# Kernel optimization log

Measured on AMD Instinct MI355X. Metric: run time of the kernel, lower is better.

The kernel has to match this reference:

```python
import jax, jax.numpy as jnp
import numpy as np
from jax import lax

B, N, T, HOR, HID = 512, 128, 128, 32, 512


def _uni(k, shape, s):
    return jax.random.uniform(k, shape, jnp.float32, -s, s)


def setup_inputs() -> dict:
    key = jax.random.key(0)
    ks = jax.random.split(key, 24)
    s = 1.0 / np.sqrt(HID)
    inp = {"window": jax.random.normal(ks[0], (B * N, T), jnp.float32)}
    # encoder LSTM (2 layers, torch gate order i,f,g,o)
    inp["Wih0"] = _uni(ks[1], (4 * HID, N), s); inp["Whh0"] = _uni(ks[2], (4 * HID, HID), s)
    inp["bih0"] = _uni(ks[3], (4 * HID,), s);   inp["bhh0"] = _uni(ks[4], (4 * HID,), s)
    inp["Wih1"] = _uni(ks[5], (4 * HID, HID), s); inp["Whh1"] = _uni(ks[6], (4 * HID, HID), s)
    inp["bih1"] = _uni(ks[7], (4 * HID,), s);     inp["bhh1"] = _uni(ks[8], (4 * HID,), s)
    # decoder cells
    inp["Wc1i"] = _uni(ks[9], (4 * HID, N), s);   inp["Wc1h"] = _uni(ks[10], (4 * HID, HID), s)
    inp["bc1i"] = _uni(ks[11], (4 * HID,), s);    inp["bc1h"] = _uni(ks[12], (4 * HID,), s)
    inp["Wc2i"] = _uni(ks[13], (4 * HID, HID), s); inp["Wc2h"] = _uni(ks[14], (4 * HID, HID), s)
    inp["bc2i"] = _uni(ks[15], (4 * HID,), s);     inp["bc2h"] = _uni(ks[16], (4 * HID,), s)
    # output projection
    inp["Wp"] = _uni(ks[17], (N, HID), s); inp["bp"] = _uni(ks[18], (N,), s)
    # deterministic inverted-dropout masks
    keep_e = 0.75  # nn.LSTM inter-layer dropout p=0.25
    keep_d = 0.8   # F.dropout p=0.2 in decode loop
    inp["enc_mask"] = (jax.random.uniform(ks[19], (T, B, HID)) < keep_e).astype(jnp.float32) / keep_e
    inp["dec_h_mask"] = (jax.random.uniform(ks[20], (HOR - 1, B, HID)) < keep_d).astype(jnp.float32) / keep_d
    inp["dec_c_mask"] = (jax.random.uniform(ks[21], (HOR - 1, B, HID)) < keep_d).astype(jnp.float32) / keep_d
    return inp


def _cell(x, h, c, Wih, Whh, bih, bhh):
    g = x @ Wih.T + h @ Whh.T + (bih + bhh)
    i, f, gg, o = jnp.split(g, 4, axis=-1)
    c = jax.nn.sigmoid(f) * c + jax.nn.sigmoid(i) * jnp.tanh(gg)
    h = jax.nn.sigmoid(o) * jnp.tanh(c)
    return h, c


def _run_layer(xs, Wih, Whh, bih, bhh):
    # xs: [T, B, D] -> outputs [T, B, HID], final (h, c)
    h0 = jnp.zeros((xs.shape[1], HID), xs.dtype)
    def step(carry, x):
        h, c = carry
        h, c = _cell(x, h, c, Wih, Whh, bih, bhh)
        return (h, c), h
    (h, c), hs = lax.scan(step, (h0, h0), xs)
    return hs, h, c


def reference(window, Wih0, Whh0, bih0, bhh0, Wih1, Whh1, bih1, bhh1,
              Wc1i, Wc1h, bc1i, bc1h, Wc2i, Wc2h, bc2i, bc2h, Wp, bp,
              enc_mask, dec_h_mask, dec_c_mask):
    x = window.reshape(B, T, N).transpose(1, 0, 2)  # [T, B, N]
    hs0, h1, c1 = _run_layer(x, Wih0, Whh0, bih0, bhh0)
    hs0 = hs0 * enc_mask  # inter-layer dropout (training mode)
    _, h2, c2 = _run_layer(hs0, Wih1, Whh1, bih1, bhh1)

    def dec_step(carry, masks):
        h1, c1, h2, c2 = carry
        mh, mc = masks
        pred = h2 @ Wp.T + bp                       # [B, N]
        h1, c1 = _cell(pred, h1, c1, Wc1i, Wc1h, bc1i, bc1h)
        h1 = h1 * mh
        c1 = c1 * mc
        h2, c2 = _cell(h1, h2, c2, Wc2i, Wc2h, bc2i, bc2h)
        return (h1, c1, h2, c2), pred

    (h1, c1, h2, c2), preds = lax.scan(dec_step, (h1, c1, h2, c2), (dec_h_mask, dec_c_mask))
    final = h2 @ Wp.T + bp                          # [B, N]
    allp = jnp.concatenate([preds, final[None]], axis=0)  # [HOR, B, N]
    # torch: each pred.view(-1,1), cat dim=1 -> [B*N, HOR]
    return allp.transpose(1, 2, 0).reshape(B * N, HOR)
```

## Files before the change

kernel.cpp:

```cpp
#include <hip/hip_runtime.h>
#include <math.h>

#define HID 512
#define BAT 512
#define NIN 128
#define TST 128
#define HOR 32
#define SBZ ((size_t)BAT * HID)
#define SL 262144
#define SLB 524288

using bf16x8 = __attribute__((ext_vector_type(8))) __bf16;
using f32x4  = __attribute__((ext_vector_type(4))) float;

__device__ __forceinline__ float sigf(float x) { return 1.0f / (1.0f + __expf(-x)); }
__device__ __forceinline__ float tanhfast(float x) { return 1.0f - 2.0f / (__expf(2.0f * x) + 1.0f); }

__device__ __forceinline__ short f2bf(float x) {
    union { float f; unsigned u; } v; v.f = x;
    unsigned r = (v.u + 0x7FFFu + ((v.u >> 16) & 1u)) >> 16;
    return (short)r;
}
__device__ __forceinline__ float bf2f(short s) {
    union { unsigned u; float f; } v; v.u = ((unsigned)(unsigned short)s) << 16;
    return v.f;
}
__device__ __forceinline__ bf16x8 asbf(f32x4 v) {
    union { f32x4 f; bf16x8 b; } u; u.f = v; return u.b;
}

__device__ __forceinline__ void pbar(unsigned* b, int sub, unsigned ep) {
    __syncthreads();
    if (threadIdx.x == 0) {
        unsigned* leaf = b + (sub >> 3) * 32;
        unsigned* root = b + 512;
        unsigned* flag = b + 544;
        unsigned old = __hip_atomic_fetch_add(leaf, 1u, __ATOMIC_RELAXED, __HIP_MEMORY_SCOPE_AGENT);
        if (old == 8u * ep - 1u) {
            unsigned ro = __hip_atomic_fetch_add(root, 1u, __ATOMIC_RELAXED, __HIP_MEMORY_SCOPE_AGENT);
            if (ro == 8u * ep - 1u)
                __hip_atomic_store(flag, ep, __ATOMIC_RELAXED, __HIP_MEMORY_SCOPE_AGENT);
        }
        int spin = 0;
        while (__hip_atomic_load(flag, __ATOMIC_RELAXED, __HIP_MEMORY_SCOPE_AGENT) < ep) {
            __builtin_amdgcn_s_sleep(1);
            if (((++spin) & 63) == 0)
                __hip_atomic_fetch_add(flag, 0u, __ATOMIC_RELAXED, __HIP_MEMORY_SCOPE_AGENT);
        }
    }
    __syncthreads();
}

__device__ __forceinline__ void gbar3(unsigned* bar, int bid, unsigned ep) {
    __syncthreads();
    if (threadIdx.x == 0) {
        unsigned* leaf = bar + ((unsigned)bid >> 3) * 32;
        unsigned* root = bar + 1024;
        unsigned* flag = bar + 1056;
        unsigned old = __hip_atomic_fetch_add(leaf, 1u, __ATOMIC_RELAXED, __HIP_MEMORY_SCOPE_AGENT);
        if (old == 8u * ep - 1u) {
            unsigned ro = __hip_atomic_fetch_add(root, 1u, __ATOMIC_RELAXED, __HIP_MEMORY_SCOPE_AGENT);
            if (ro == 32u * ep - 1u)
                __hip_atomic_store(flag, ep, __ATOMIC_RELAXED, __HIP_MEMORY_SCOPE_AGENT);
        }
        int spin = 0;
        while (__hip_atomic_load(flag, __ATOMIC_RELAXED, __HIP_MEMORY_SCOPE_AGENT) < ep) {
            __builtin_amdgcn_s_sleep(1);
            if (((++spin) & 63) == 0)
                __hip_atomic_fetch_add(flag, 0u, __ATOMIC_RELAXED, __HIP_MEMORY_SCOPE_AGENT);
        }
    }
    __syncthreads();
}


__global__ __launch_bounds__(256) void prep_w(const float* __restrict__ Wih,
                                              const float* __restrict__ Whh,
                                              short* __restrict__ W2, int Kx, int Kp) {
    size_t i = (size_t)blockIdx.x * 256 + threadIdx.x;
    if (i >= (size_t)2048 * Kp) return;
    int np = (int)(i / Kp), kp = (int)(i % Kp);
    int u = np >> 2, gate = np & 3;
    int on = gate * HID + u;
    float w = (kp < Kx) ? Wih[(size_t)on * Kx + kp] : Whh[(size_t)on * HID + (kp - Kx)];
    W2[i] = f2bf(w);
}

__global__ __launch_bounds__(256) void prep_x(const float* __restrict__ window,
                                              short* __restrict__ X2t) {
    size_t i = (size_t)blockIdx.x * 256 + threadIdx.x;
    if (i >= (size_t)TST * BAT * NIN) return;
    int n = (int)(i & 127);
    int b = (int)((i >> 7) & 511);
    int t = (int)(i >> 16);
    float x = window[(size_t)b * (TST * NIN) + (size_t)t * NIN + n];
    int rg = b >> 4;
    int l = (b & 15) + (((n >> 3) & 3) << 4);
    int e = n & 7;
    size_t base = (size_t)t * 65536 + ((size_t)(rg * 4 + (n >> 5)) << 9) + l * 8 + e;
    X2t[base] = f2bf(x);
}

__global__ __launch_bounds__(256) void prep_fuse(const float* __restrict__ Wc1i,
                                                 const float* __restrict__ Wp,
                                                 float* __restrict__ Wfuse) {
    size_t i = (size_t)blockIdx.x * 256 + threadIdx.x;
    if (i >= (size_t)2048 * 512) return;
    int on = (int)(i >> 9), k = (int)(i & 511);
    float s = 0.f;
    for (int n = 0; n < NIN; ++n) s += Wc1i[(size_t)on * NIN + n] * Wp[(size_t)n * HID + k];
    Wfuse[i] = s;
}

__global__ __launch_bounds__(256) void prep_badd(const float* __restrict__ Wc1i,
                                                 const float* __restrict__ bp,
                                                 float* __restrict__ badd) {
    int on = blockIdx.x * 256 + threadIdx.x;
    if (on >= 2048) return;
    float s = 0.f;
    for (int n = 0; n < NIN; ++n) s += Wc1i[(size_t)on * NIN + n] * bp[n];
    badd[on] = s;
}

__global__ __launch_bounds__(256) void prep_bias(const float* __restrict__ bih,
                                                 const float* __restrict__ bhh,
                                                 const float* __restrict__ badd,
                                                 float* __restrict__ bout) {
    int np = blockIdx.x * 256 + threadIdx.x;
    if (np >= 2048) return;
    int on = (np & 3) * HID + (np >> 2);
    float v = bih[on] + bhh[on];
    if (badd) v += badd[on];
    bout[np] = v;
}

__global__ __launch_bounds__(256) void prep_wp(const float* __restrict__ Wp,
                                               short* __restrict__ W2p) {
    int i = blockIdx.x * 256 + threadIdx.x;
    if (i >= 128 * 512) return;
    W2p[i] = f2bf(Wp[i]);
}


template<bool SC>
__device__ __forceinline__ void gl16(f32x4& q, const char* p) {
    if constexpr (SC)
        asm volatile("global_load_dwordx4 %0, %1, off sc0 sc1" : "=v"(q) : "v"(p));
    else
        asm volatile("global_load_dwordx4 %0, %1, off" : "=v"(q) : "v"(p));
}

__device__ __forceinline__ void load_wres32(char* lds, const short* Wg, int K) {
    const int tid = threadIdx.x;
    const int r = tid >> 4;
    const int cnt = K >> 7;
    const int jb = (tid & 15) * cnt;
    for (int q = 0; q < cnt; ++q) {
        int j = jb + q;
        bf16x8 v = *(const bf16x8*)(Wg + (size_t)r * K + j * 8);
        *(bf16x8*)(lds + j * 512 + r * 16) = v;
    }
}

__device__ __forceinline__ void load_wres64(char* lds, const short* Wg, int K) {
    const int r = threadIdx.x >> 2, jg = threadIdx.x & 3;
    for (int q = 0; q < (K >> 5); ++q) {
        int j = jg + (q << 2);
        bf16x8 v = *(const bf16x8*)(Wg + (size_t)r * K + j * 8);
        *(bf16x8*)(lds + (size_t)j * 1024 + r * 16) = v;
    }
}

__device__ __forceinline__ void pre_mask_asm(const float* msk, int mrow, int u0, float o[4]) {
    const int lane = threadIdx.x & 63;
    const float* p = msk + (size_t)(mrow + ((lane >> 3) << 2)) * HID + u0 + (lane & 7);
#pragma unroll
    for (int r = 0; r < 4; ++r)
        asm volatile("global_load_dword %0, %1, off" : "=v"(o[r]) : "v"(p + (size_t)r * HID));
}

template<int C0, int C1, bool SC0, bool SC1>
__device__ __forceinline__ void gemm64(
    const char* wres, const short* a0t, const short* a1t,
    int mb, f32x4 acc[2][4])
{
    constexpr int NKC = C0 + C1;
    constexpr int D = 16;
    const int lane = threadIdx.x & 63;
    const int arow = lane & 15, akg = lane >> 4;
    const size_t lb = (size_t)lane << 4;
    const char* base0 = (const char*)a0t;
    const char* base1 = (const char*)a1t;
    auto cptr = [&](int kc, int fh) -> const char* {
        return (kc < C0)
            ? base0 + (((size_t)(mb * 2 + fh) * C0 + kc) << 10) + lb
            : base1 + (((size_t)(mb * 2 + fh) * C1 + (kc - C0)) << 10) + lb;
    };
    f32x4 q0[D], q1[D];
#pragma unroll
    for (int i = 0; i < D; ++i) {
        if (i < C0) { gl16<SC0>(q0[i], cptr(i, 0)); gl16<SC0>(q1[i], cptr(i, 1)); }
        else        { gl16<SC1>(q0[i], cptr(i, 0)); gl16<SC1>(q1[i], cptr(i, 1)); }
    }
#pragma unroll
    for (int kc = 0; kc < NKC; ++kc) {
        const int sl = kc % D;
        asm volatile("s_waitcnt vmcnt(%2)"
                     : "+v"(q0[sl]), "+v"(q1[sl])
                     : "i"((2 * ((NKC - kc) < D ? (NKC - kc) : D)) - 2));
        const bf16x8 fa0 = asbf(q0[sl]);
        const bf16x8 fa1 = asbf(q1[sl]);
        if (kc + D < NKC) {
            if (kc + D < C0) { gl16<SC0>(q0[sl], cptr(kc + D, 0)); gl16<SC0>(q1[sl], cptr(kc + D, 1)); }
            else             { gl16<SC1>(q0[sl], cptr(kc + D, 0)); gl16<SC1>(q1[sl], cptr(kc + D, 1)); }
        }
        const char* wrow = wres + (size_t)((kc << 2) + akg) * 1024;
        bf16x8 fb[4];
#pragma unroll
        for (int nj = 0; nj < 4; ++nj)
            fb[nj] = *(const bf16x8*)(wrow + ((nj * 16 + arow) << 4));
#pragma unroll
        for (int nj = 0; nj < 4; ++nj) {
            acc[0][nj] = __builtin_amdgcn_mfma_f32_16x16x32_bf16(fa0, fb[nj], acc[0][nj], 0, 0, 0);
            acc[1][nj] = __builtin_amdgcn_mfma_f32_16x16x32_bf16(fa1, fb[nj], acc[1][nj], 0, 0, 0);
        }
    }
    asm volatile("s_waitcnt vmcnt(0)");
}

__device__ __forceinline__ void cell_epi64(
    char* scrw, f32x4 acc[2][4], float creg[2][4], int mb, int np0,
    const float* bias_p, const float* mh, const float* mc, const float* ma,
    short* h_out, short* h_aux)
{
    const int lane = threadIdx.x & 63;
#pragma unroll
    for (int p = 0; p < 2; ++p) {
        const int np0p = np0 + (p << 5);
#pragma unroll
        for (int mi = 0; mi < 2; ++mi)
#pragma unroll
            for (int nj = 0; nj < 2; ++nj) {
                const int row = mi * 16 + ((lane >> 4) << 2);
                const int col = nj * 16 + (lane & 15);
#pragma unroll
                for (int r = 0; r < 4; ++r)
                    *(float*)(scrw + (row + r) * 128 + (col << 2)) = acc[mi][p * 2 + nj][r];
            }
        asm volatile("s_waitcnt lgkmcnt(0)" ::: "memory");
        const int ul = lane & 7, g = lane >> 3;
        f32x4 gv[4];
#pragma unroll
        for (int r = 0; r < 4; ++r)
            gv[r] = *(const f32x4*)(scrw + ((g << 2) + r) * 128 + (ul << 4));
        asm volatile("s_waitcnt lgkmcnt(0)" ::: "memory");
        const float4 bs = *(const float4*)(bias_p + np0p + (ul << 2));
#pragma unroll
        for (int r = 0; r < 4; ++r) {
            const int m = (g << 2) + r;
            const int fh = m >> 4, r16 = m & 15;
            const float gi = gv[r][0] + bs.x, gf = gv[r][1] + bs.y;
            const float gg = gv[r][2] + bs.z, go = gv[r][3] + bs.w;
            const float cn = sigf(gf) * creg[p][r] + sigf(gi) * tanhfast(gg);
            const float h  = sigf(go) * tanhfast(cn);
            creg[p][r] = mc ? cn * mc[p * 4 + r] : cn;
            const float hm = mh ? h * mh[p * 4 + r] : h;
            const int idx2 = (r16 << 3) + ul;
            *(short*)(scrw + fh * 256 + idx2 * 2) = f2bf(hm);
            if (h_aux)
                *(short*)(scrw + 512 + fh * 256 + idx2 * 2) = f2bf(h * ma[p * 4 + r]);
        }
        const int u0p = np0p >> 2;
        const int c_hi = u0p >> 5, gsub = (u0p >> 3) & 3;
        unsigned vmain[2], vaux[2];
#pragma unroll
        for (int s = 0; s < 2; ++s)
            vmain[s] = *(const unsigned*)(scrw + s * 256 + (lane << 2));
        if (h_aux)
#pragma unroll
            for (int s = 0; s < 2; ++s)
                vaux[s] = *(const unsigned*)(scrw + 512 + s * 256 + (lane << 2));
        asm volatile("s_waitcnt lgkmcnt(0)" ::: "memory");
#pragma unroll
        for (int s = 0; s < 2; ++s) {
            const unsigned* dst = (const unsigned*)(h_out
                + ((size_t)((mb * 2 + s) * 16 + c_hi) << 9) + (gsub << 7)) + lane;
            asm volatile("global_store_dword %0, %1, off sc0 sc1" :: "v"(dst), "v"(vmain[s]));
        }
        if (h_aux)
#pragma unroll
            for (int s = 0; s < 2; ++s) {
                const unsigned* dst = (const unsigned*)(h_aux
                    + ((size_t)((mb * 2 + s) * 16 + c_hi) << 9) + (gsub << 7)) + lane;
                asm volatile("global_store_dword %0, %1, off sc0 sc1" :: "v"(dst), "v"(vaux[s]));
            }
    }
}


__global__ void __launch_bounds__(256, 1) persist_kernel(
    const short* __restrict__ X2t,
    const short* __restrict__ W0, const short* __restrict__ W1,
    const short* __restrict__ Wd1, const short* __restrict__ Wd2,
    short* hA0, short* hA1, short* hd0, short* hd1, short* hB0, short* hB1,
    short* hBall0, short* hBallR,
    const float* __restrict__ bias0, const float* __restrict__ bias1,
    const float* __restrict__ biasd1, const float* __restrict__ biasd2,
    const float* __restrict__ enc_mask, const float* __restrict__ dec_h_mask,
    const float* __restrict__ dec_c_mask, unsigned* bar)
{
    extern __shared__ __align__(16) char lds[];
    const int bid = blockIdx.x;
    const int xcd = bid & 7;
    const int half = xcd >> 2;
    const int mtile = xcd & 3;
    const int m0 = mtile * 128;
    const int ntile = bid >> 3;
    const int np0 = ntile * 64;
    const int u0 = np0 >> 2;
    const int w = threadIdx.x >> 6;
    const int mb = (m0 >> 5) + w;
    const int mrow = m0 + (w << 5);
    char* scrw = lds + 131072 + (w << 12);
    float creg[2][4] = {{0.f,0.f,0.f,0.f},{0.f,0.f,0.f,0.f}};

    unsigned* pb = bar + mtile * 1024;
    unsigned* gb = bar + 4096;
    const int sub = (half << 5) | ntile;

    auto hA_rd = [&](int t) -> const short* { return (t & 1) ? hA1 : hA0; };
    auto hA_wr = [&](int t) -> short* { return (t & 1) ? hA0 : hA1; };
    auto hd_at = [&](int t) -> short* { return (t & 1) ? hd1 : hd0; };
    auto hB_rd = [&](int t) -> const short* { return (t & 1) ? hB1 : hB0; };
    auto hB_wr = [&](int t) -> short* { return (t & 1) ? hB0 : hB1; };
    auto decA_at = [&](int i) -> short* { return (i & 1) ? hA1 : hA0; };
    auto hball = [&](int i) -> short* { return (i == 0) ? hBall0 : hBallR + (size_t)(i - 1) * SL; };

    load_wres64(lds, (half ? W1 : W0) + (size_t)np0 * (half ? 1024 : 640), half ? 1024 : 640);
    __syncthreads();
    unsigned ep = 0;
    for (int tt = 0; tt <= TST; ++tt) {
        if (half == 0) {
            if (tt < TST) {
                const int t = tt;
                float ma[8];
                pre_mask_asm(enc_mask + (size_t)t * SBZ, mrow, u0, ma);
                pre_mask_asm(enc_mask + (size_t)t * SBZ, mrow, u0 + 8, ma + 4);
                f32x4 acc[2][4];
#pragma unroll
                for (int a = 0; a < 2; ++a)
#pragma unroll
                    for (int b2 = 0; b2 < 4; ++b2) acc[a][b2] = (f32x4){0.f, 0.f, 0.f, 0.f};
                gemm64<4, 16, false, true>(lds, X2t + (size_t)t * 65536, hA_rd(t), mb, acc);
                cell_epi64(scrw, acc, creg, mb, np0, bias0, nullptr, nullptr, ma,
                           hA_wr(t), hd_at(t));
            }
        } else {
            if (tt >= 1) {
                const int t = tt - 1;
                f32x4 acc[2][4];
#pragma unroll
                for (int a = 0; a < 2; ++a)
#pragma unroll
                    for (int b2 = 0; b2 < 4; ++b2) acc[a][b2] = (f32x4){0.f, 0.f, 0.f, 0.f};
                gemm64<16, 16, true, true>(lds, hd_at(t), hB_rd(t), mb, acc);
                short* outp = (t == TST - 1) ? hBall0 : hB_wr(t);
                cell_epi64(scrw, acc, creg, mb, np0, bias1, nullptr, nullptr, nullptr,
                           outp, nullptr);
            }
        }
        pbar(pb, sub, ++ep);
    }

    gbar3(gb, bid, 1u);

    load_wres64(lds, (half ? Wd2 : Wd1) + (size_t)np0 * 1024, 1024);
    __syncthreads();
    for (int s = 0; s < HOR - 1; ++s) {
        if (half == 0) {
            float mh[8], mc[8];
            pre_mask_asm(dec_h_mask + (size_t)s * SBZ, mrow, u0, mh);
            pre_mask_asm(dec_h_mask + (size_t)s * SBZ, mrow, u0 + 8, mh + 4);
            pre_mask_asm(dec_c_mask + (size_t)s * SBZ, mrow, u0, mc);
            pre_mask_asm(dec_c_mask + (size_t)s * SBZ, mrow, u0 + 8, mc + 4);
            f32x4 acc[2][4];
#pragma unroll
            for (int a = 0; a < 2; ++a)
#pragma unroll
                for (int b2 = 0; b2 < 4; ++b2) acc[a][b2] = (f32x4){0.f, 0.f, 0.f, 0.f};
            gemm64<16, 16, true, true>(lds, hball(s), decA_at(s), mb, acc);
            cell_epi64(scrw, acc, creg, mb, np0, biasd1, mh, mc, nullptr,
                       decA_at(s + 1), nullptr);
        }
        pbar(pb, sub, ++ep);
        if (half == 1) {
            f32x4 acc[2][4];
#pragma unroll
            for (int a = 0; a < 2; ++a)
#pragma unroll
                for (int b2 = 0; b2 < 4; ++b2) acc[a][b2] = (f32x4){0.f, 0.f, 0.f, 0.f};
            gemm64<16, 16, true, true>(lds, decA_at(s + 1), hball(s), mb, acc);
            cell_epi64(scrw, acc, creg, mb, np0, biasd2, nullptr, nullptr, nullptr,
                       hball(s + 1), nullptr);
        }
        pbar(pb, sub, ++ep);
    }
}


template<int C0, int C1>
__device__ __forceinline__ void gemm_pipeP(
    const char* wres, const short* a0t, const short* a1t,
    int mb, f32x4 acc[2][2])
{
    constexpr int NKC = C0 + C1;
    constexpr int D = 16;
    const int lane = threadIdx.x & 63;
    const int arow = lane & 15, akg = lane >> 4;
    const size_t lb = (size_t)lane << 4;
    const char* base0 = (const char*)a0t;
    const char* base1 = (const char*)a1t;
    auto cptr = [&](int kc, int fh) -> const char* {
        return (kc < C0)
            ? base0 + (((size_t)(mb * 2 + fh) * C0 + kc) << 10) + lb
            : base1 + (((size_t)(mb * 2 + fh) * C1 + (kc - C0)) << 10) + lb;
    };
    f32x4 q0[D], q1[D];
#pragma unroll
    for (int i = 0; i < D; ++i) {
        gl16<false>(q0[i], cptr(i, 0));
        gl16<false>(q1[i], cptr(i, 1));
    }
#pragma unroll
    for (int kc = 0; kc < NKC; ++kc) {
        const int sl = kc % D;
        asm volatile("s_waitcnt vmcnt(%2)"
                     : "+v"(q0[sl]), "+v"(q1[sl])
                     : "i"((2 * ((NKC - kc) < D ? (NKC - kc) : D)) - 2));
        const bf16x8 fa0 = asbf(q0[sl]);
        const bf16x8 fa1 = asbf(q1[sl]);
        if (kc + D < NKC) {
            gl16<false>(q0[sl], cptr(kc + D, 0));
            gl16<false>(q1[sl], cptr(kc + D, 1));
        }
        const char* wrow = wres + (size_t)(((kc << 2) + akg) << 9);
        const bf16x8 fb0 = *(const bf16x8*)(wrow + (arow << 4));
        const bf16x8 fb1 = *(const bf16x8*)(wrow + ((16 + arow) << 4));
        acc[0][0] = __builtin_amdgcn_mfma_f32_16x16x32_bf16(fa0, fb0, acc[0][0], 0, 0, 0);
        acc[0][1] = __builtin_amdgcn_mfma_f32_16x16x32_bf16(fa0, fb1, acc[0][1], 0, 0, 0);
        acc[1][0] = __builtin_amdgcn_mfma_f32_16x16x32_bf16(fa1, fb0, acc[1][0], 0, 0, 0);
        acc[1][1] = __builtin_amdgcn_mfma_f32_16x16x32_bf16(fa1, fb1, acc[1][1], 0, 0, 0);
    }
    asm volatile("s_waitcnt vmcnt(0)");
}

__global__ void __launch_bounds__(512, 2) proj_kernel(
    const short* hBall0, const short* hBallR, const short* __restrict__ W2p,
    const float* __restrict__ bp, float* __restrict__ pred_all)
{
    extern __shared__ __align__(16) char lds[];
    const int bid = blockIdx.x;
    const int s = bid >> 3, q = bid & 7;
    const int bh = q >> 2, n0p = (q & 3) * 32;
    load_wres32(lds, W2p + (size_t)n0p * 512, 512);
    const int w = threadIdx.x >> 6, lane = threadIdx.x & 63;
    char* scrw = lds + 32768 + w * 4608;
    const int mb = bh * 8 + w;
    const short* A = (s == 0) ? hBall0 : hBallR + (size_t)(s - 1) * SL;
    __syncthreads();
    f32x4 acc[2][2];
#pragma unroll
    for (int a = 0; a < 2; ++a)
#pragma unroll
        for (int b2 = 0; b2 < 2; ++b2) acc[a][b2] = (f32x4){0.f, 0.f, 0.f, 0.f};
    gemm_pipeP<16, 0>(lds, A, A, mb, acc);
#pragma unroll
    for (int mi = 0; mi < 2; ++mi)
#pragma unroll
        for (int ni = 0; ni < 2; ++ni) {
            const int row = mi * 16 + ((lane >> 4) << 2);
            const int col = ni * 16 + (lane & 15);
#pragma unroll
            for (int r = 0; r < 4; ++r)
                *(float*)(scrw + (row + r) * 144 + (col << 2)) = acc[mi][ni][r];
        }
    asm volatile("s_waitcnt lgkmcnt(0)" ::: "memory");
    const int rr = lane >> 1, hf = lane & 1;
    float* dst = pred_all + (size_t)s * (BAT * NIN)
               + (size_t)(bh * 256 + w * 32 + rr) * NIN + n0p + hf * 16;
#pragma unroll
    for (int t4 = 0; t4 < 4; ++t4) {
        f32x4 v = *(const f32x4*)(scrw + rr * 144 + hf * 64 + t4 * 16);
        const float4 b4 = *(const float4*)(bp + n0p + hf * 16 + t4 * 4);
        v[0] += b4.x; v[1] += b4.y; v[2] += b4.z; v[3] += b4.w;
        *(f32x4*)(dst + t4 * 4) = v;
    }
}

__global__ __launch_bounds__(256) void transpose_out(const float* __restrict__ pred_all,
                                                     float* __restrict__ out) {
    __shared__ float tl[32][65];
    const int base = blockIdx.x * 64;
    const int tid = threadIdx.x;
    for (int i = tid; i < 32 * 64; i += 256) {
        int s = i >> 6, f = i & 63;
        tl[s][f] = pred_all[(size_t)s * (BAT * NIN) + base + f];
    }
    __syncthreads();
    for (int i = tid; i < 64 * 32; i += 256) {
        int f = i >> 5, s = i & 31;
        out[(size_t)(base + f) * HOR + s] = tl[s][f];
    }
}


extern "C" void kernel_launch(void* const* d_in, const int* in_sizes, int n_in,
                              void* d_out, int out_size, void* d_ws, size_t ws_size,
                              hipStream_t stream) {
    (void)in_sizes; (void)n_in; (void)out_size; (void)ws_size;
    const float* window = (const float*)d_in[0];
    const float* Wih0 = (const float*)d_in[1];
    const float* Whh0 = (const float*)d_in[2];
    const float* bih0 = (const float*)d_in[3];
    const float* bhh0 = (const float*)d_in[4];
    const float* Wih1 = (const float*)d_in[5];
    const float* Whh1 = (const float*)d_in[6];
    const float* bih1 = (const float*)d_in[7];
    const float* bhh1 = (const float*)d_in[8];
    const float* Wc1i = (const float*)d_in[9];
    const float* Wc1h = (const float*)d_in[10];
    const float* bc1i = (const float*)d_in[11];
    const float* bc1h = (const float*)d_in[12];
    const float* Wc2i = (const float*)d_in[13];
    const float* Wc2h = (const float*)d_in[14];
    const float* bc2i = (const float*)d_in[15];
    const float* bc2h = (const float*)d_in[16];
    const float* Wp   = (const float*)d_in[17];
    const float* bp   = (const float*)d_in[18];
    const float* enc_mask   = (const float*)d_in[19];
    const float* dec_h_mask = (const float*)d_in[20];
    const float* dec_c_mask = (const float*)d_in[21];
    float* out = (float*)d_out;

    char* base = (char*)d_ws;
    size_t off = 0;
    auto take = [&](size_t bytes) -> char* {
        off = (off + 255) & ~(size_t)255;
        char* r = base + off; off += bytes; return r;
    };
    short* W2e0 = (short*)take((size_t)2048 * 640 * 2);
    short* W2e1 = (short*)take((size_t)2048 * 1024 * 2);
    short* W2d1 = (short*)take((size_t)2048 * 1024 * 2);
    short* W2d2 = (short*)take((size_t)2048 * 1024 * 2);
    short* W2p  = (short*)take((size_t)128 * 512 * 2);
    float* Wfuse = (float*)take((size_t)2048 * 512 * 4);
    float* badd  = (float*)take((size_t)2048 * 4);
    float* bias0 = (float*)take((size_t)2048 * 4);
    float* bias1 = (float*)take((size_t)2048 * 4);
    float* biasd1 = (float*)take((size_t)2048 * 4);
    float* biasd2 = (float*)take((size_t)2048 * 4);
    short* hBall0 = (short*)take(SLB);
    float* pred_all = (float*)take((size_t)HOR * BAT * NIN * 4);
    unsigned* bars = (unsigned*)take(32768);
    short* X2t = (short*)take((size_t)TST * 65536 * 2);
    short* hA0 = (short*)take(SLB);
    short* hA1 = (short*)take(SLB);
    short* hd0 = (short*)take(SLB);
    short* hd1 = (short*)take(SLB);
    short* hB0 = (short*)take(SLB);
    short* hB1 = (short*)take(SLB);
    short* hBallR = X2t;

    prep_fuse<<<(2048 * 512 + 255) / 256, 256, 0, stream>>>(Wc1i, Wp, Wfuse);
    prep_badd<<<8, 256, 0, stream>>>(Wc1i, bp, badd);
    prep_wp<<<(128 * 512 + 255) / 256, 256, 0, stream>>>(Wp, W2p);
    prep_w<<<(2048 * 640 + 255) / 256, 256, 0, stream>>>(Wih0, Whh0, W2e0, NIN, 640);
    prep_w<<<(2048 * 1024 + 255) / 256, 256, 0, stream>>>(Wih1, Whh1, W2e1, HID, 1024);
    prep_w<<<(2048 * 1024 + 255) / 256, 256, 0, stream>>>(Wfuse, Wc1h, W2d1, HID, 1024);
    prep_w<<<(2048 * 1024 + 255) / 256, 256, 0, stream>>>(Wc2i, Wc2h, W2d2, HID, 1024);
    prep_bias<<<8, 256, 0, stream>>>(bih0, bhh0, nullptr, bias0);
    prep_bias<<<8, 256, 0, stream>>>(bih1, bhh1, nullptr, bias1);
    prep_bias<<<8, 256, 0, stream>>>(bc1i, bc1h, badd, biasd1);
    prep_bias<<<8, 256, 0, stream>>>(bc2i, bc2h, nullptr, biasd2);
    prep_x<<<(int)(((size_t)TST * BAT * NIN + 255) / 256), 256, 0, stream>>>(window, X2t);
    hipMemsetAsync(hA0, 0, SLB, stream);
    hipMemsetAsync(hB0, 0, SLB, stream);
    hipMemsetAsync(bars, 0, 32768, stream);

    hipFuncSetAttribute((const void*)&persist_kernel,
                        hipFuncAttributeMaxDynamicSharedMemorySize, 163840);
    persist_kernel<<<256, 256, 147456, stream>>>(
        X2t, W2e0, W2e1, W2d1, W2d2,
        hA0, hA1, hd0, hd1, hB0, hB1,
        hBall0, hBallR,
        bias0, bias1, biasd1, biasd2,
        enc_mask, dec_h_mask, dec_c_mask, bars);

    hipFuncSetAttribute((const void*)&proj_kernel,
                        hipFuncAttributeMaxDynamicSharedMemorySize, 69632);
    proj_kernel<<<256, 512, 69632, stream>>>(hBall0, hBallR, W2p, bp, pred_all);

    transpose_out<<<(BAT * NIN) / 64, 256, 0, stream>>>(pred_all, out);
}
```

Baseline: 1.736 ms.

## Replace coherent hidden-state loads with 16-slot ring buffers and periodic acquire fences

Hidden-state buffers for the encoder and decoder are changed from double buffers to 16-deep ring buffers, so each step reads a fresh address. That lets the recurrent GEMM loads drop the sc0/sc1 cache-bypass bits and use normal cached loads. Coherence now comes from an agent-scope acquire fence issued once every 16 barrier epochs, which invalidates stale cache lines before any ring slot is reused. The cost is more memory footprint, and correctness depends on the fence cadence lining up with ring reuse.

```diff
diff --git a/kernel.cpp b/kernel.cpp
--- a/kernel.cpp
+++ b/kernel.cpp
@@ -142,12 +142,8 @@
 }
 
 
-template<bool SC>
-__device__ __forceinline__ void gl16(f32x4& q, const char* p) {
-    if constexpr (SC)
-        asm volatile("global_load_dwordx4 %0, %1, off sc0 sc1" : "=v"(q) : "v"(p));
-    else
-        asm volatile("global_load_dwordx4 %0, %1, off" : "=v"(q) : "v"(p));
+__device__ __forceinline__ void gl16c(f32x4& q, const char* p) {
+    asm volatile("global_load_dwordx4 %0, %1, off" : "=v"(q) : "v"(p));
 }
 
 __device__ __forceinline__ void load_wres32(char* lds, const short* Wg, int K) {
@@ -179,7 +175,7 @@
         asm volatile("global_load_dword %0, %1, off" : "=v"(o[r]) : "v"(p + (size_t)r * HID));
 }
 
-template<int C0, int C1, bool SC0, bool SC1>
+template<int C0, int C1>
 __device__ __forceinline__ void gemm64(
     const char* wres, const short* a0t, const short* a1t,
     int mb, f32x4 acc[2][4])
@@ -199,8 +195,8 @@
     f32x4 q0[D], q1[D];
 #pragma unroll
     for (int i = 0; i < D; ++i) {
-        if (i < C0) { gl16<SC0>(q0[i], cptr(i, 0)); gl16<SC0>(q1[i], cptr(i, 1)); }
-        else        { gl16<SC1>(q0[i], cptr(i, 0)); gl16<SC1>(q1[i], cptr(i, 1)); }
+        gl16c(q0[i], cptr(i, 0));
+        gl16c(q1[i], cptr(i, 1));
     }
 #pragma unroll
     for (int kc = 0; kc < NKC; ++kc) {
@@ -211,8 +207,8 @@
         const bf16x8 fa0 = asbf(q0[sl]);
         const bf16x8 fa1 = asbf(q1[sl]);
         if (kc + D < NKC) {
-            if (kc + D < C0) { gl16<SC0>(q0[sl], cptr(kc + D, 0)); gl16<SC0>(q1[sl], cptr(kc + D, 1)); }
-            else             { gl16<SC1>(q0[sl], cptr(kc + D, 0)); gl16<SC1>(q1[sl], cptr(kc + D, 1)); }
+            gl16c(q0[sl], cptr(kc + D, 0));
+            gl16c(q1[sl], cptr(kc + D, 1));
         }
         const char* wrow = wres + (size_t)((kc << 2) + akg) * 1024;
         bf16x8 fb[4];
@@ -302,7 +298,7 @@
     const short* __restrict__ X2t,
     const short* __restrict__ W0, const short* __restrict__ W1,
     const short* __restrict__ Wd1, const short* __restrict__ Wd2,
-    short* hA0, short* hA1, short* hd0, short* hd1, short* hB0, short* hB1,
+    short* hAring, short* hdring, short* hBring, short* decAring,
     short* hBall0, short* hBallR,
     const float* __restrict__ bias0, const float* __restrict__ bias1,
     const float* __restrict__ biasd1, const float* __restrict__ biasd2,
@@ -328,12 +324,14 @@
     unsigned* gb = bar + 4096;
     const int sub = (half << 5) | ntile;
 
-    auto hA_rd = [&](int t) -> const short* { return (t & 1) ? hA1 : hA0; };
-    auto hA_wr = [&](int t) -> short* { return (t & 1) ? hA0 : hA1; };
-    auto hd_at = [&](int t) -> short* { return (t & 1) ? hd1 : hd0; };
-    auto hB_rd = [&](int t) -> const short* { return (t & 1) ? hB1 : hB0; };
-    auto hB_wr = [&](int t) -> short* { return (t & 1) ? hB0 : hB1; };
-    auto decA_at = [&](int i) -> short* { return (i & 1) ? hA1 : hA0; };
+    auto hA_rd = [&](int t) -> const short* { return hAring + (size_t)(t & 15) * SL; };
+    auto hA_wr = [&](int t) -> short* { return hAring + (size_t)((t + 1) & 15) * SL; };
+    auto hd_at = [&](int t) -> short* { return hdring + (size_t)(t & 15) * SL; };
+    auto hB_rd = [&](int t) -> const short* { return hBring + (size_t)(t & 15) * SL; };
+    auto hB_wr = [&](int t) -> short* { return hBring + (size_t)((t + 1) & 15) * SL; };
+    auto decA_at = [&](int i) -> short* {
+        return (i == 0) ? hAring : decAring + (size_t)(i & 15) * SL;
+    };
     auto hball = [&](int i) -> short* { return (i == 0) ? hBall0 : hBallR + (size_t)(i - 1) * SL; };
 
     load_wres64(lds, (half ? W1 : W0) + (size_t)np0 * (half ? 1024 : 640), half ? 1024 : 640);
@@ -351,7 +349,7 @@
                 for (int a = 0; a < 2; ++a)
 #pragma unroll
                     for (int b2 = 0; b2 < 4; ++b2) acc[a][b2] = (f32x4){0.f, 0.f, 0.f, 0.f};
-                gemm64<4, 16, false, true>(lds, X2t + (size_t)t * 65536, hA_rd(t), mb, acc);
+                gemm64<4, 16>(lds, X2t + (size_t)t * 65536, hA_rd(t), mb, acc);
                 cell_epi64(scrw, acc, creg, mb, np0, bias0, nullptr, nullptr, ma,
                            hA_wr(t), hd_at(t));
             }
@@ -363,16 +361,19 @@
                 for (int a = 0; a < 2; ++a)
 #pragma unroll
                     for (int b2 = 0; b2 < 4; ++b2) acc[a][b2] = (f32x4){0.f, 0.f, 0.f, 0.f};
-                gemm64<16, 16, true, true>(lds, hd_at(t), hB_rd(t), mb, acc);
+                gemm64<16, 16>(lds, hd_at(t), hB_rd(t), mb, acc);
                 short* outp = (t == TST - 1) ? hBall0 : hB_wr(t);
                 cell_epi64(scrw, acc, creg, mb, np0, bias1, nullptr, nullptr, nullptr,
                            outp, nullptr);
             }
         }
         pbar(pb, sub, ++ep);
+        if ((ep & 15) == 2)
+            __builtin_amdgcn_fence(__ATOMIC_ACQUIRE, "agent");
     }
 
     gbar3(gb, bid, 1u);
+    __builtin_amdgcn_fence(__ATOMIC_ACQUIRE, "agent");
 
     load_wres64(lds, (half ? Wd2 : Wd1) + (size_t)np0 * 1024, 1024);
     __syncthreads();
@@ -388,22 +389,26 @@
             for (int a = 0; a < 2; ++a)
 #pragma unroll
                 for (int b2 = 0; b2 < 4; ++b2) acc[a][b2] = (f32x4){0.f, 0.f, 0.f, 0.f};
-            gemm64<16, 16, true, true>(lds, hball(s), decA_at(s), mb, acc);
+            gemm64<16, 16>(lds, hball(s), decA_at(s), mb, acc);
             cell_epi64(scrw, acc, creg, mb, np0, biasd1, mh, mc, nullptr,
                        decA_at(s + 1), nullptr);
         }
         pbar(pb, sub, ++ep);
+        if ((ep & 15) == 2)
+            __builtin_amdgcn_fence(__ATOMIC_ACQUIRE, "agent");
         if (half == 1) {
             f32x4 acc[2][4];
 #pragma unroll
             for (int a = 0; a < 2; ++a)
 #pragma unroll
                 for (int b2 = 0; b2 < 4; ++b2) acc[a][b2] = (f32x4){0.f, 0.f, 0.f, 0.f};
-            gemm64<16, 16, true, true>(lds, decA_at(s + 1), hball(s), mb, acc);
+            gemm64<16, 16>(lds, decA_at(s + 1), hball(s), mb, acc);
             cell_epi64(scrw, acc, creg, mb, np0, biasd2, nullptr, nullptr, nullptr,
                        hball(s + 1), nullptr);
         }
         pbar(pb, sub, ++ep);
+        if ((ep & 15) == 2)
+            __builtin_amdgcn_fence(__ATOMIC_ACQUIRE, "agent");
     }
 }
 
@@ -428,8 +433,8 @@
     f32x4 q0[D], q1[D];
 #pragma unroll
     for (int i = 0; i < D; ++i) {
-        gl16<false>(q0[i], cptr(i, 0));
-        gl16<false>(q1[i], cptr(i, 1));
+        gl16c(q0[i], cptr(i, 0));
+        gl16c(q1[i], cptr(i, 1));
     }
 #pragma unroll
     for (int kc = 0; kc < NKC; ++kc) {
@@ -440,8 +445,8 @@
         const bf16x8 fa0 = asbf(q0[sl]);
         const bf16x8 fa1 = asbf(q1[sl]);
         if (kc + D < NKC) {
-            gl16<false>(q0[sl], cptr(kc + D, 0));
-            gl16<false>(q1[sl], cptr(kc + D, 1));
+            gl16c(q0[sl], cptr(kc + D, 0));
+            gl16c(q1[sl], cptr(kc + D, 1));
         }
         const char* wrow = wres + (size_t)(((kc << 2) + akg) << 9);
         const bf16x8 fb0 = *(const bf16x8*)(wrow + (arow << 4));
@@ -563,12 +568,10 @@
     float* pred_all = (float*)take((size_t)HOR * BAT * NIN * 4);
     unsigned* bars = (unsigned*)take(32768);
     short* X2t = (short*)take((size_t)TST * 65536 * 2);
-    short* hA0 = (short*)take(SLB);
-    short* hA1 = (short*)take(SLB);
-    short* hd0 = (short*)take(SLB);
-    short* hd1 = (short*)take(SLB);
-    short* hB0 = (short*)take(SLB);
-    short* hB1 = (short*)take(SLB);
+    short* hAring  = (short*)take((size_t)16 * SLB);
+    short* hdring  = (short*)take((size_t)16 * SLB);
+    short* hBring  = (short*)take((size_t)16 * SLB);
+    short* decAring = (short*)take((size_t)16 * SLB);
     short* hBallR = X2t;
 
     prep_fuse<<<(2048 * 512 + 255) / 256, 256, 0, stream>>>(Wc1i, Wp, Wfuse);
@@ -583,15 +586,15 @@
     prep_bias<<<8, 256, 0, stream>>>(bc1i, bc1h, badd, biasd1);
     prep_bias<<<8, 256, 0, stream>>>(bc2i, bc2h, nullptr, biasd2);
     prep_x<<<(int)(((size_t)TST * BAT * NIN + 255) / 256), 256, 0, stream>>>(window, X2t);
-    hipMemsetAsync(hA0, 0, SLB, stream);
-    hipMemsetAsync(hB0, 0, SLB, stream);
+    hipMemsetAsync(hAring, 0, SLB, stream);
+    hipMemsetAsync(hBring, 0, SLB, stream);
     hipMemsetAsync(bars, 0, 32768, stream);
 
     hipFuncSetAttribute((const void*)&persist_kernel,
                         hipFuncAttributeMaxDynamicSharedMemorySize, 163840);
     persist_kernel<<<256, 256, 147456, stream>>>(
         X2t, W2e0, W2e1, W2d1, W2d2,
-        hA0, hA1, hd0, hd1, hB0, hB1,
+        hAring, hdring, hBring, decAring,
         hBall0, hBallR,
         bias0, bias1, biasd1, biasd2,
         enc_mask, dec_h_mask, dec_c_mask, bars);
```

Result: slower. 1.840 ms (+6.0%).
